# Performance work log

Measured on AMD Instinct MI355X. Metric: run time of the kernel, lower is better.

Reference implementation:

```python
import jax, jax.numpy as jnp
import numpy as np

N_QUBITS = 8
N_LAYERS = 3
BATCH = 8192


def setup_inputs() -> dict:
    key = jax.random.key(0)
    k0, k1, k2, k3 = jax.random.split(key, 4)
    return {
        "x": jax.random.normal(k0, (BATCH, N_QUBITS), jnp.float32),
        "quantum_weights": jax.random.normal(k1, (N_LAYERS, N_QUBITS, 2), jnp.float32) * 0.1,
        "W1": jax.random.normal(k2, (N_QUBITS, 64), jnp.float32) / np.float32(np.sqrt(N_QUBITS)),
        "b1": jnp.zeros((64,), jnp.float32),
        "W2": jax.random.normal(k3, (64, 256), jnp.float32) / np.float32(np.sqrt(64)),
        "b2": jnp.zeros((256,), jnp.float32),
    }


def _ry(theta):
    # RY(t) = [[cos t/2, -sin t/2], [sin t/2, cos t/2]]; theta: [] or [B]
    c = jnp.cos(theta * 0.5)
    s = jnp.sin(theta * 0.5)
    U = jnp.stack([jnp.stack([c, -s], axis=-1), jnp.stack([s, c], axis=-1)], axis=-2)
    return U.astype(jnp.complex64)


def _rz(theta):
    # RZ(t) = diag(e^{-it/2}, e^{it/2})
    em = jnp.exp(-0.5j * theta.astype(jnp.complex64))
    ep = jnp.exp(0.5j * theta.astype(jnp.complex64))
    z = jnp.zeros_like(em)
    return jnp.stack([jnp.stack([em, z], axis=-1), jnp.stack([z, ep], axis=-1)], axis=-2)


def _apply_1q(state, U, q):
    # state: [B, 2,2,...,2]; qubit q lives on axis q+1. U: [2,2] (shared) or [B,2,2].
    s = jnp.moveaxis(state, q + 1, -1)
    if U.ndim == 3:
        s = jnp.einsum('b...i,bji->b...j', s, U)
    else:
        s = jnp.einsum('b...i,ji->b...j', s, U)
    return jnp.moveaxis(s, -1, q + 1)


def _cnot(state, c, t):
    # flip target bit on the control=1 slice
    s = jnp.moveaxis(state, (c + 1, t + 1), (1, 2))
    s = jnp.stack([s[:, 0], s[:, 1, ::-1]], axis=1)
    return jnp.moveaxis(s, (1, 2), (c + 1, t + 1))


def _quantum_forward(x, qw):
    B = x.shape[0]
    xmin = x.min(axis=1, keepdims=True)
    xmax = x.max(axis=1, keepdims=True)
    xn = (x - xmin) / (xmax - xmin + 1e-8)
    # |0...0> state, shape [B, 2]*n
    state = jnp.zeros((B,) + (2,) * N_QUBITS, jnp.complex64)
    state = state.at[(slice(None),) + (0,) * N_QUBITS].set(1.0)
    # feature encoding: RY(x_norm * pi), per-sample angles
    for q in range(N_QUBITS):
        state = _apply_1q(state, _ry(xn[:, q] * jnp.pi), q)
    # variational layers
    for layer in range(N_LAYERS):
        for q in range(N_QUBITS):
            state = _apply_1q(state, _ry(qw[layer, q, 0]), q)
            state = _apply_1q(state, _rz(qw[layer, q, 1]), q)
        for q in range(N_QUBITS):
            state = _cnot(state, q, (q + 1) % N_QUBITS)
    probs = jnp.real(state * jnp.conj(state))  # [B, 2]*n, float32
    z = []
    for q in range(N_QUBITS):
        p = probs.sum(axis=tuple(a for a in range(1, N_QUBITS + 1) if a != q + 1))
        z.append(p[:, 0] - p[:, 1])  # <Z_q>
    return jnp.stack(z, axis=1)  # [B, n_qubits]


def reference(x, quantum_weights, W1, b1, W2, b2):
    z = _quantum_forward(x, quantum_weights).astype(jnp.float32)
    h = jax.nn.relu(z @ W1 + b1)
    return h @ W2 + b2
```

## Files before the change

### kernel.cpp

```cpp
#include <hip/hip_runtime.h>

#define NQ 8
#define NLAYERS 3

typedef unsigned int uint2ev __attribute__((ext_vector_type(2)));
typedef float f2 __attribute__((ext_vector_type(2)));
typedef __attribute__((address_space(3))) unsigned int lds_u32;
typedef __attribute__((address_space(1))) const unsigned int glb_u32;

template<int MASK>
__device__ __forceinline__ float xorlane(float v, int r) {
    if constexpr (MASK == 1) {
        return __int_as_float(__builtin_amdgcn_mov_dpp(__float_as_int(v), 0xB1, 0xF, 0xF, false));
    } else if constexpr (MASK == 2) {
        return __int_as_float(__builtin_amdgcn_mov_dpp(__float_as_int(v), 0x4E, 0xF, 0xF, false));
    } else if constexpr (MASK == 4) {
        return __int_as_float(__builtin_amdgcn_ds_swizzle(__float_as_int(v), 0x101F));
    } else if constexpr (MASK == 8) {
        return __int_as_float(__builtin_amdgcn_mov_dpp(__float_as_int(v), 0x128, 0xF, 0xF, false));
    }
}

template<int MASK>
__device__ __forceinline__ f2 xorlane2(f2 v, int r) {
    f2 o;
    o.x = xorlane<MASK>(v.x, r);
    o.y = xorlane<MASK>(v.y, r);
    return o;
}

template<int CTRL>
__device__ __forceinline__ float dpp_add_stage(float v) {
    int moved = __builtin_amdgcn_update_dpp(0, __float_as_int(v), CTRL, 0xF, 0xF, false);
    return v + __int_as_float(moved);
}
__device__ __forceinline__ float rowsum15(float v) {
    v = dpp_add_stage<0x111>(v);
    v = dpp_add_stage<0x112>(v);
    v = dpp_add_stage<0x114>(v);
    v = dpp_add_stage<0x118>(v);
    return v;
}

__device__ __forceinline__ float bcast15(float v) {
    return __int_as_float(__builtin_amdgcn_ds_swizzle(__float_as_int(v), 0x1F0));
}

__device__ __forceinline__ f2 cmul(f2 a, f2 b) {
    f2 r;
    r.x = a.x * b.x - a.y * b.y;
    r.y = a.x * b.y + a.y * b.x;
    return r;
}

__device__ __forceinline__ f2 splat(float c) { f2 v; v.x = c; v.y = c; return v; }

template<int Q>
__device__ __forceinline__ void ry16(float c, float s, f2 A[16], int r) {
    f2 vc = splat(c), vs = splat(s);
    if constexpr (Q < 4) {
        constexpr int M = 1 << Q;
#pragma unroll
        for (int j = 0; j < 16; ++j) if (!(j & M)) {
            f2 a0 = A[j], a1 = A[j | M];
            A[j]     = vc * a0 - vs * a1;
            A[j | M] = vs * a0 + vc * a1;
        }
    } else {
        constexpr int LM = 1 << (Q - 4);
        f2 vsg = (r & LM) ? vs : (splat(0.f) - vs);
#pragma unroll
        for (int j = 0; j < 16; ++j) {
            f2 p = xorlane2<LM>(A[j], r);
            A[j] = vc * A[j] + vsg * p;
        }
    }
}

__device__ __forceinline__ void ry16_q7_relab(float c, float s, f2 A[16], int r) {
    f2 vc = splat(c), vs = splat(s);
    f2 vsg = (r & 8) ? vs : (splat(0.f) - vs);
#pragma unroll
    for (int m = 0; m < 8; ++m) {
        f2 pa = xorlane2<8>(A[2 * m + 1], r);
        f2 pb = xorlane2<8>(A[2 * m],     r);
        A[2 * m]     = vc * A[2 * m]     + vsg * pa;
        A[2 * m + 1] = vc * A[2 * m + 1] + vsg * pb;
    }
}

__device__ __forceinline__ void ring16(f2 A[16], int lane, int r) {
    f2 t;
    t = A[1]; A[1] = A[3]; A[3] = t;
    t = A[5]; A[5] = A[7]; A[7] = t;
    t = A[9]; A[9] = A[11]; A[11] = t;
    t = A[13]; A[13] = A[15]; A[15] = t;
    t = A[2]; A[2] = A[6]; A[6] = t;
    t = A[3]; A[3] = A[7]; A[7] = t;
    t = A[10]; A[10] = A[14]; A[14] = t;
    t = A[11]; A[11] = A[15]; A[15] = t;
    t = A[4]; A[4] = A[12]; A[12] = t;
    t = A[5]; A[5] = A[13]; A[13] = t;
    t = A[6]; A[6] = A[14]; A[14] = t;
    t = A[7]; A[7] = A[15]; A[15] = t;

    int sA = ((lane & 48) | ((r ^ (r << 1)) & 15)) << 2;
    int sB = sA ^ 4;
#pragma unroll
    for (int j = 0; j < 8; ++j) {
        A[j].x = __int_as_float(__builtin_amdgcn_ds_bpermute(sA, __float_as_int(A[j].x)));
        A[j].y = __int_as_float(__builtin_amdgcn_ds_bpermute(sA, __float_as_int(A[j].y)));
    }
#pragma unroll
    for (int j = 8; j < 16; ++j) {
        A[j].x = __int_as_float(__builtin_amdgcn_ds_bpermute(sB, __float_as_int(A[j].x)));
        A[j].y = __int_as_float(__builtin_amdgcn_ds_bpermute(sB, __float_as_int(A[j].y)));
    }
}

__global__ __launch_bounds__(256) void qfused(
    const float* __restrict__ x,
    const float* __restrict__ qw,
    const float* __restrict__ W1,
    const float* __restrict__ b1,
    const float* __restrict__ W2,
    const float* __restrict__ b2,
    float* __restrict__ out,
    int B)
{
    __shared__ float4 tab[NLAYERS * NQ];
    __shared__ float h_lds[16][64];
    __shared__ float w2_lds[64 * 256];

    int tid = threadIdx.x;
    if (tid < NLAYERS * NQ) {
        float w0 = 0.5f * qw[tid * 2 + 0];
        float w1 = 0.5f * qw[tid * 2 + 1];
        if (tid < 8)
            tab[tid] = make_float4(w0, 0.f, __cosf(w1), __sinf(w1));
        else
            tab[tid] = make_float4(__cosf(w0), __sinf(w0), __cosf(w1), __sinf(w1));
    }

    int lane = tid & 63;
    int wid  = tid >> 6;
    int g    = lane >> 4;
    int r    = lane & 15;
    int sl   = wid * 4 + g;
    int sbase = blockIdx.x * 16;
    int sample = sbase + sl;
    if (sample >= B) sample = B - 1;

    const float4* x4 = (const float4*)(x + sample * 8);
    float4 xa = x4[0], xb = x4[1];

    __syncthreads();

#pragma unroll
    for (int k = 0; k < 16; ++k) {
        int row = wid * 16 + k;
        __builtin_amdgcn_global_load_lds(
            (glb_u32*)(W2 + row * 256 + lane * 4),
            (lds_u32*)&w2_lds[row * 256],
            16, 0, 0);
    }

    float xs[8] = {xa.x, xa.y, xa.z, xa.w, xb.x, xb.y, xb.z, xb.w};
    float xmin = xs[0], xmax = xs[0];
#pragma unroll
    for (int q = 1; q < 8; ++q) {
        xmin = fminf(xmin, xs[q]);
        xmax = fmaxf(xmax, xs[q]);
    }
    float inv_pi2 = 1.5707963267948966f / (xmax - xmin + 1e-8f);

    float4 T8 = tab[8],  T9 = tab[9],  T10 = tab[10], T11 = tab[11];
    float4 T12 = tab[12], T13 = tab[13], T14 = tab[14], T15 = tab[15];
    float4 T16 = tab[16], T17 = tab[17], T18 = tab[18], T19 = tab[19];
    float4 T20 = tab[20], T21 = tab[21], T22 = tab[22], T23 = tab[23];

    float cc[8], ss[8], cw[8], sw[8];
#pragma unroll
    for (int q = 0; q < 8; ++q) {
        float4 t0 = tab[q];
        float a = fmaf(xs[q] - xmin, inv_pi2, t0.x);
        __sincosf(a, &ss[q], &cc[q]);
        cw[q] = t0.z;
        sw[q] = t0.w;
    }

    int r0v = r & 1, r3v = (r >> 3) & 1;

    f2 X0[2], X1[2], X2[2], X3[2], X4[2];
#pragma unroll
    for (int k = 0; k < 2; ++k) {
        { int b = k ^ r3v; float rr = b ? ss[0] : cc[0];
          X0[k].x = rr * cw[0]; X0[k].y = (b ? rr : -rr) * sw[0]; }
        { int b = k ^ r3v; float rr = b ? ss[1] : cc[1];
          X1[k].x = rr * cw[1]; X1[k].y = (b ? rr : -rr) * sw[1]; }
        { int b = k;        float rr = b ? ss[2] : cc[2];
          X2[k].x = rr * cw[2]; X2[k].y = (b ? rr : -rr) * sw[2]; }
        { int b = k;        float rr = b ? ss[3] : cc[3];
          X3[k].x = rr * cw[3]; X3[k].y = (b ? rr : -rr) * sw[3]; }
        { int b = k ^ r0v;  float rr = b ? ss[4] : cc[4];
          X4[k].x = rr * cw[4]; X4[k].y = (b ? rr : -rr) * sw[4]; }
    }

    f2 pl;
    {
        int b5 = (r ^ (r >> 1)) & 1;
        int b6 = ((r >> 1) ^ (r >> 2)) & 1;
        int b7 = ((r >> 2) ^ (r >> 3)) & 1;
        f2 f5, f6, f7;
        float r5 = b5 ? ss[5] : cc[5];
        f5.x = r5 * cw[5]; f5.y = (b5 ? r5 : -r5) * sw[5];
        float r6 = b6 ? ss[6] : cc[6];
        f6.x = r6 * cw[6]; f6.y = (b6 ? r6 : -r6) * sw[6];
        float r7 = b7 ? ss[7] : cc[7];
        f7.x = r7 * cw[7]; f7.y = (b7 ? r7 : -r7) * sw[7];
        pl = cmul(cmul(f5, f6), f7);
    }

    f2 PP[2][2];
    {
        f2 t0 = cmul(pl, X0[0]);
        f2 t1 = cmul(pl, X0[1]);
        PP[0][0] = cmul(t0, X1[0]);
        PP[0][1] = cmul(t0, X1[1]);
        PP[1][0] = cmul(t1, X1[1]);
        PP[1][1] = cmul(t1, X1[0]);
    }
    f2 Q34[2][2];
    Q34[0][0] = cmul(X3[0], X4[0]);
    Q34[0][1] = cmul(X3[1], X4[1]);
    Q34[1][0] = cmul(X3[1], X4[0]);
    Q34[1][1] = cmul(X3[0], X4[1]);
    f2 R[2][2][2];
#pragma unroll
    for (int j1 = 0; j1 < 2; ++j1)
#pragma unroll
        for (int j2 = 0; j2 < 2; ++j2)
#pragma unroll
            for (int j3 = 0; j3 < 2; ++j3)
                R[j1][j2][j3] = cmul(X2[j1 ^ j2], Q34[j2][j3]);

    f2 A[16];
#pragma unroll
    for (int j3 = 0; j3 < 2; ++j3)
#pragma unroll
        for (int j2 = 0; j2 < 2; ++j2)
#pragma unroll
            for (int j1 = 0; j1 < 2; ++j1)
#pragma unroll
                for (int j0 = 0; j0 < 2; ++j0) {
                    int j = j0 + 2 * j1 + 4 * j2 + 8 * j3;
                    A[j] = cmul(PP[j0][j1], R[j1][j2][j3]);
                }

    ry16<0>(T8.x,  T8.y,  A, r);
    ry16<1>(T9.x,  T9.y,  A, r);
    ry16<2>(T10.x, T10.y, A, r);
    ry16<3>(T11.x, T11.y, A, r);
    ry16<4>(T12.x, T12.y, A, r);
    ry16<5>(T13.x, T13.y, A, r);
    ry16<6>(T14.x, T14.y, A, r);
    ry16<7>(T15.x, T15.y, A, r);

    {
        f2 L;
        {
            f2 d4, d5, d6, d7;
            d4.x = T12.z; d4.y = (r & 1) ? T12.w : -T12.w;
            d5.x = T13.z; d5.y = (r & 2) ? T13.w : -T13.w;
            d6.x = T14.z; d6.y = (r & 4) ? T14.w : -T14.w;
            d7.x = T15.z; d7.y = (r & 8) ? T15.w : -T15.w;
            L = cmul(cmul(d4, d5), cmul(d6, d7));
        }
        f2 d0n, d0p, d1n, d1p, d2n, d2p, d3n, d3p;
        d0n.x = T8.z;  d0n.y = -T8.w;   d0p.x = T8.z;  d0p.y = T8.w;
        d1n.x = T9.z;  d1n.y = -T9.w;   d1p.x = T9.z;  d1p.y = T9.w;
        d2n.x = T10.z; d2n.y = -T10.w;  d2p.x = T10.z; d2p.y = T10.w;
        d3n.x = T11.z; d3n.y = -T11.w;  d3p.x = T11.z; d3p.y = T11.w;

        f2 t01[4];
        {
            f2 l0 = cmul(L, d0n), l1 = cmul(L, d0p);
            t01[0] = cmul(l0, d1n);
            t01[1] = cmul(l1, d1n);
            t01[2] = cmul(l0, d1p);
            t01[3] = cmul(l1, d1p);
        }
        f2 m23[4];
        m23[0] = cmul(d2n, d3n);
        m23[1] = cmul(d2p, d3n);
        m23[2] = cmul(d2n, d3p);
        m23[3] = cmul(d2p, d3p);

#pragma unroll
        for (int j = 0; j < 16; ++j) {
            f2 D = cmul(t01[j & 3], m23[j >> 2]);
            A[j] = cmul(A[j], D);
        }
    }

    ring16(A, lane, r);

    {
        float s0l2 = (r & 8) ? -T16.y : T16.y;
        ry16<0>(T16.x, s0l2, A, r);
    }
    ry16<1>(T17.x, T17.y, A, r);
    ry16<2>(T18.x, T18.y, A, r);
    ry16<3>(T19.x, T19.y, A, r);
    ry16<4>(T20.x, T20.y, A, r);
    ry16<5>(T21.x, T21.y, A, r);
    ry16<6>(T22.x, T22.y, A, r);
    ry16_q7_relab(T23.x, T23.y, A, r);

    float P[16];
#pragma unroll
    for (int j = 0; j < 16; ++j) P[j] = A[j].x * A[j].x + A[j].y * A[j].y;

    float Sp[8], Dp[8];
#pragma unroll
    for (int k = 0; k < 8; ++k) {
        Sp[k] = P[2 * k] + P[2 * k + 1];
        Dp[k] = P[2 * k] - P[2 * k + 1];
    }
    float U0 = ((Sp[0] - Sp[1]) - (Sp[2] - Sp[3])) - ((Sp[4] - Sp[5]) - (Sp[6] - Sp[7]));
    float U3 = ((Dp[0] - Dp[1]) - (Dp[2] - Dp[3])) - ((Dp[4] - Dp[5]) - (Dp[6] - Dp[7]));
    float U1 = (Dp[0] - Dp[1]) + (Dp[2] - Dp[3]) + (Dp[4] - Dp[5]) + (Dp[6] - Dp[7]);
    float U2 = ((Dp[0] - Dp[1]) - (Dp[2] - Dp[3])) + ((Dp[4] - Dp[5]) - (Dp[6] - Dp[7]));

    {
        float sg73 = (r & 8) ? -1.f : 1.f;
        U1 *= sg73; U2 *= sg73; U3 *= sg73;
    }

    int p1 = r & 1;
    int p2 = (r ^ (r >> 1)) & 1;
    int p3 = (r ^ (r >> 1) ^ (r >> 2)) & 1;
    int p4 = (r ^ (r >> 1) ^ (r >> 2) ^ (r >> 3)) & 1;

    float z0 = bcast15(rowsum15(p4 ? -U0 : U0));
    float z1 = bcast15(rowsum15(U1));
    float z2 = bcast15(rowsum15(U2));
    float z3 = bcast15(rowsum15(U3));
    float z4 = bcast15(rowsum15(p1 ? -U3 : U3));
    float z5 = bcast15(rowsum15(p2 ? -U3 : U3));
    float z6 = bcast15(rowsum15(p3 ? -U3 : U3));
    float z7 = bcast15(rowsum15(p4 ? -U3 : U3));

    {
        int c0 = r * 4;
        f2 accL = *(const f2*)(b1 + c0);
        f2 accH = *(const f2*)(b1 + c0 + 2);
        const float* w1p = W1 + c0;
        float zq[8] = {z0, z1, z2, z3, z4, z5, z6, z7};
#pragma unroll
        for (int q = 0; q < 8; ++q) {
            f2 wL = *(const f2*)(w1p + q * 64);
            f2 wH = *(const f2*)(w1p + q * 64 + 2);
            f2 zz = splat(zq[q]);
            accL = accL + zz * wL;
            accH = accH + zz * wH;
        }
        accL.x = fmaxf(accL.x, 0.f); accL.y = fmaxf(accL.y, 0.f);
        accH.x = fmaxf(accH.x, 0.f); accH.y = fmaxf(accH.y, 0.f);
        *(float4*)&h_lds[sl][c0] = make_float4(accL.x, accL.y, accH.x, accH.y);
    }
    __syncthreads();

    int sg = tid >> 6;
    int c4 = (tid & 63) * 4;
    f2 bbL = *(const f2*)(b2 + c4);
    f2 bbH = *(const f2*)(b2 + c4 + 2);
    f2 a0L = bbL, a0H = bbH, a1L = bbL, a1H = bbH;
    f2 a2L = bbL, a2H = bbH, a3L = bbL, a3H = bbH;
    const int sO = sg * 4;

#pragma unroll 2
    for (int i4 = 0; i4 < 16; ++i4) {
        const float* wrow = &w2_lds[i4 * 4 * 256 + c4];
        f2 w0L = *(const f2*)(wrow);        f2 w0H = *(const f2*)(wrow + 2);
        f2 w1L = *(const f2*)(wrow + 256);  f2 w1H = *(const f2*)(wrow + 258);
        f2 w2L = *(const f2*)(wrow + 512);  f2 w2H = *(const f2*)(wrow + 514);
        f2 w3L = *(const f2*)(wrow + 768);  f2 w3H = *(const f2*)(wrow + 770);
        float4 h0 = *(const float4*)&h_lds[sO + 0][i4 * 4];
        float4 h1 = *(const float4*)&h_lds[sO + 1][i4 * 4];
        float4 h2 = *(const float4*)&h_lds[sO + 2][i4 * 4];
        float4 h3 = *(const float4*)&h_lds[sO + 3][i4 * 4];

        a0L = a0L + splat(h0.x) * w0L + splat(h0.y) * w1L + splat(h0.z) * w2L + splat(h0.w) * w3L;
        a0H = a0H + splat(h0.x) * w0H + splat(h0.y) * w1H + splat(h0.z) * w2H + splat(h0.w) * w3H;
        a1L = a1L + splat(h1.x) * w0L + splat(h1.y) * w1L + splat(h1.z) * w2L + splat(h1.w) * w3L;
        a1H = a1H + splat(h1.x) * w0H + splat(h1.y) * w1H + splat(h1.z) * w2H + splat(h1.w) * w3H;
        a2L = a2L + splat(h2.x) * w0L + splat(h2.y) * w1L + splat(h2.z) * w2L + splat(h2.w) * w3L;
        a2H = a2H + splat(h2.x) * w0H + splat(h2.y) * w1H + splat(h2.z) * w2H + splat(h2.w) * w3H;
        a3L = a3L + splat(h3.x) * w0L + splat(h3.y) * w1L + splat(h3.z) * w2L + splat(h3.w) * w3L;
        a3H = a3H + splat(h3.x) * w0H + splat(h3.y) * w1H + splat(h3.z) * w2H + splat(h3.w) * w3H;
    }

    int srow = sbase + sO;
    if (srow + 0 < B) *(float4*)(out + (srow + 0) * 256 + c4) = make_float4(a0L.x, a0L.y, a0H.x, a0H.y);
    if (srow + 1 < B) *(float4*)(out + (srow + 1) * 256 + c4) = make_float4(a1L.x, a1L.y, a1H.x, a1H.y);
    if (srow + 2 < B) *(float4*)(out + (srow + 2) * 256 + c4) = make_float4(a2L.x, a2L.y, a2H.x, a2H.y);
    if (srow + 3 < B) *(float4*)(out + (srow + 3) * 256 + c4) = make_float4(a3L.x, a3L.y, a3H.x, a3H.y);
}

extern "C" void kernel_launch(void* const* d_in, const int* in_sizes, int n_in,
                              void* d_out, int out_size, void* d_ws, size_t ws_size,
                              hipStream_t stream) {
    const float* x  = (const float*)d_in[0];
    const float* qw = (const float*)d_in[1];
    const float* W1 = (const float*)d_in[2];
    const float* b1 = (const float*)d_in[3];
    const float* W2 = (const float*)d_in[4];
    const float* b2 = (const float*)d_in[5];
    float* out = (float*)d_out;

    int B = in_sizes[0] / NQ;

    qfused<<<(B + 15) / 16, 256, 0, stream>>>(x, qw, W1, b1, W2, b2, out, B);
}
```

Before: 17.97 us.

## Process two samples per 16-lane group and halve block size to 128 threads

Each 16-lane group now simulates two samples' statevectors interleaved, so the block needs 128 threads instead of 256 while still covering 16 samples. The state-building, rotation, measurement and dense layers are factored into helpers called twice, which gives more instruction-level parallelism per thread. Each thread's W2 LDS load count doubles and the second GEMM accumulates 8 rows per thread. The cost is higher register pressure and fewer waves per block, which may reduce latency hiding.

After: 19.57 us. +8.9%, slower.

```diff
diff --git a/kernel.cpp b/kernel.cpp
--- a/kernel.cpp
+++ b/kernel.cpp
@@ -118,7 +118,168 @@
     }
 }
 
-__global__ __launch_bounds__(256) void qfused(
+__device__ __forceinline__ void build_state(const float xs[8], const float4* tab,
+                                            int r, f2 A[16]) {
+    float xmin = xs[0], xmax = xs[0];
+#pragma unroll
+    for (int q = 1; q < 8; ++q) {
+        xmin = fminf(xmin, xs[q]);
+        xmax = fmaxf(xmax, xs[q]);
+    }
+    float inv_pi2 = 1.5707963267948966f / (xmax - xmin + 1e-8f);
+
+    float cc[8], ss[8], cw[8], sw[8];
+#pragma unroll
+    for (int q = 0; q < 8; ++q) {
+        float4 t0 = tab[q];
+        float a = fmaf(xs[q] - xmin, inv_pi2, t0.x);
+        __sincosf(a, &ss[q], &cc[q]);
+        cw[q] = t0.z;
+        sw[q] = t0.w;
+    }
+
+    int r0v = r & 1, r3v = (r >> 3) & 1;
+
+    f2 X0[2], X1[2], X2[2], X3[2], X4[2];
+#pragma unroll
+    for (int k = 0; k < 2; ++k) {
+        { int b = k ^ r3v; float rr = b ? ss[0] : cc[0];
+          X0[k].x = rr * cw[0]; X0[k].y = (b ? rr : -rr) * sw[0]; }
+        { int b = k ^ r3v; float rr = b ? ss[1] : cc[1];
+          X1[k].x = rr * cw[1]; X1[k].y = (b ? rr : -rr) * sw[1]; }
+        { int b = k;        float rr = b ? ss[2] : cc[2];
+          X2[k].x = rr * cw[2]; X2[k].y = (b ? rr : -rr) * sw[2]; }
+        { int b = k;        float rr = b ? ss[3] : cc[3];
+          X3[k].x = rr * cw[3]; X3[k].y = (b ? rr : -rr) * sw[3]; }
+        { int b = k ^ r0v;  float rr = b ? ss[4] : cc[4];
+          X4[k].x = rr * cw[4]; X4[k].y = (b ? rr : -rr) * sw[4]; }
+    }
+
+    f2 pl;
+    {
+        int b5 = (r ^ (r >> 1)) & 1;
+        int b6 = ((r >> 1) ^ (r >> 2)) & 1;
+        int b7 = ((r >> 2) ^ (r >> 3)) & 1;
+        f2 f5, f6, f7;
+        float r5 = b5 ? ss[5] : cc[5];
+        f5.x = r5 * cw[5]; f5.y = (b5 ? r5 : -r5) * sw[5];
+        float r6 = b6 ? ss[6] : cc[6];
+        f6.x = r6 * cw[6]; f6.y = (b6 ? r6 : -r6) * sw[6];
+        float r7 = b7 ? ss[7] : cc[7];
+        f7.x = r7 * cw[7]; f7.y = (b7 ? r7 : -r7) * sw[7];
+        pl = cmul(cmul(f5, f6), f7);
+    }
+
+    f2 PP[2][2];
+    {
+        f2 t0 = cmul(pl, X0[0]);
+        f2 t1 = cmul(pl, X0[1]);
+        PP[0][0] = cmul(t0, X1[0]);
+        PP[0][1] = cmul(t0, X1[1]);
+        PP[1][0] = cmul(t1, X1[1]);
+        PP[1][1] = cmul(t1, X1[0]);
+    }
+    f2 Q34[2][2];
+    Q34[0][0] = cmul(X3[0], X4[0]);
+    Q34[0][1] = cmul(X3[1], X4[1]);
+    Q34[1][0] = cmul(X3[1], X4[0]);
+    Q34[1][1] = cmul(X3[0], X4[1]);
+    f2 R[2][2][2];
+#pragma unroll
+    for (int j1 = 0; j1 < 2; ++j1)
+#pragma unroll
+        for (int j2 = 0; j2 < 2; ++j2)
+#pragma unroll
+            for (int j3 = 0; j3 < 2; ++j3)
+                R[j1][j2][j3] = cmul(X2[j1 ^ j2], Q34[j2][j3]);
+
+#pragma unroll
+    for (int j3 = 0; j3 < 2; ++j3)
+#pragma unroll
+        for (int j2 = 0; j2 < 2; ++j2)
+#pragma unroll
+            for (int j1 = 0; j1 < 2; ++j1)
+#pragma unroll
+                for (int j0 = 0; j0 < 2; ++j0) {
+                    int j = j0 + 2 * j1 + 4 * j2 + 8 * j3;
+                    A[j] = cmul(PP[j0][j1], R[j1][j2][j3]);
+                }
+}
+
+__device__ __forceinline__ void rz1_diag(const float4* tab, int r, f2 A[16]) {
+    float4 T12 = tab[12], T13 = tab[13], T14 = tab[14], T15 = tab[15];
+    float4 T8 = tab[8], T9 = tab[9], T10 = tab[10], T11 = tab[11];
+    f2 L;
+    {
+        f2 d4, d5, d6, d7;
+        d4.x = T12.z; d4.y = (r & 1) ? T12.w : -T12.w;
+        d5.x = T13.z; d5.y = (r & 2) ? T13.w : -T13.w;
+        d6.x = T14.z; d6.y = (r & 4) ? T14.w : -T14.w;
+        d7.x = T15.z; d7.y = (r & 8) ? T15.w : -T15.w;
+        L = cmul(cmul(d4, d5), cmul(d6, d7));
+    }
+    f2 d0n, d0p, d1n, d1p, d2n, d2p, d3n, d3p;
+    d0n.x = T8.z;  d0n.y = -T8.w;   d0p.x = T8.z;  d0p.y = T8.w;
+    d1n.x = T9.z;  d1n.y = -T9.w;   d1p.x = T9.z;  d1p.y = T9.w;
+    d2n.x = T10.z; d2n.y = -T10.w;  d2p.x = T10.z; d2p.y = T10.w;
+    d3n.x = T11.z; d3n.y = -T11.w;  d3p.x = T11.z; d3p.y = T11.w;
+
+    f2 t01[4];
+    {
+        f2 l0 = cmul(L, d0n), l1 = cmul(L, d0p);
+        t01[0] = cmul(l0, d1n);
+        t01[1] = cmul(l1, d1n);
+        t01[2] = cmul(l0, d1p);
+        t01[3] = cmul(l1, d1p);
+    }
+    f2 m23[4];
+    m23[0] = cmul(d2n, d3n);
+    m23[1] = cmul(d2p, d3n);
+    m23[2] = cmul(d2n, d3p);
+    m23[3] = cmul(d2p, d3p);
+
+#pragma unroll
+    for (int j = 0; j < 16; ++j) {
+        f2 D = cmul(t01[j & 3], m23[j >> 2]);
+        A[j] = cmul(A[j], D);
+    }
+}
+
+__device__ __forceinline__ void measure16(const f2 A[16], int r, float z[8]) {
+    float P[16];
+#pragma unroll
+    for (int j = 0; j < 16; ++j) P[j] = A[j].x * A[j].x + A[j].y * A[j].y;
+
+    float Sp[8], Dp[8];
+#pragma unroll
+    for (int k = 0; k < 8; ++k) {
+        Sp[k] = P[2 * k] + P[2 * k + 1];
+        Dp[k] = P[2 * k] - P[2 * k + 1];
+    }
+    float U0 = ((Sp[0] - Sp[1]) - (Sp[2] - Sp[3])) - ((Sp[4] - Sp[5]) - (Sp[6] - Sp[7]));
+    float U3 = ((Dp[0] - Dp[1]) - (Dp[2] - Dp[3])) - ((Dp[4] - Dp[5]) - (Dp[6] - Dp[7]));
+    float U1 = (Dp[0] - Dp[1]) + (Dp[2] - Dp[3]) + (Dp[4] - Dp[5]) + (Dp[6] - Dp[7]);
+    float U2 = ((Dp[0] - Dp[1]) - (Dp[2] - Dp[3])) + ((Dp[4] - Dp[5]) - (Dp[6] - Dp[7]));
+
+    float sg73 = (r & 8) ? -1.f : 1.f;
+    U1 *= sg73; U2 *= sg73; U3 *= sg73;
+
+    int p1 = r & 1;
+    int p2 = (r ^ (r >> 1)) & 1;
+    int p3 = (r ^ (r >> 1) ^ (r >> 2)) & 1;
+    int p4 = (r ^ (r >> 1) ^ (r >> 2) ^ (r >> 3)) & 1;
+
+    z[0] = bcast15(rowsum15(p4 ? -U0 : U0));
+    z[1] = bcast15(rowsum15(U1));
+    z[2] = bcast15(rowsum15(U2));
+    z[3] = bcast15(rowsum15(U3));
+    z[4] = bcast15(rowsum15(p1 ? -U3 : U3));
+    z[5] = bcast15(rowsum15(p2 ? -U3 : U3));
+    z[6] = bcast15(rowsum15(p3 ? -U3 : U3));
+    z[7] = bcast15(rowsum15(p4 ? -U3 : U3));
+}
+
+__global__ __launch_bounds__(128) void qfused(
     const float* __restrict__ x,
     const float* __restrict__ qw,
     const float* __restrict__ W1,
@@ -146,238 +307,105 @@
     int wid  = tid >> 6;
     int g    = lane >> 4;
     int r    = lane & 15;
-    int sl   = wid * 4 + g;
+    int slA  = wid * 8 + g;
+    int slB  = slA + 4;
     int sbase = blockIdx.x * 16;
-    int sample = sbase + sl;
-    if (sample >= B) sample = B - 1;
-
-    const float4* x4 = (const float4*)(x + sample * 8);
-    float4 xa = x4[0], xb = x4[1];
+    int sampleA = sbase + slA; if (sampleA >= B) sampleA = B - 1;
+    int sampleB = sbase + slB; if (sampleB >= B) sampleB = B - 1;
+
+    const float4* xA4 = (const float4*)(x + sampleA * 8);
+    float4 xa0 = xA4[0], xa1 = xA4[1];
+    const float4* xB4 = (const float4*)(x + sampleB * 8);
+    float4 xb0 = xB4[0], xb1 = xB4[1];
 
     __syncthreads();
 
 #pragma unroll
-    for (int k = 0; k < 16; ++k) {
-        int row = wid * 16 + k;
+    for (int k = 0; k < 32; ++k) {
+        int row = wid * 32 + k;
         __builtin_amdgcn_global_load_lds(
             (glb_u32*)(W2 + row * 256 + lane * 4),
             (lds_u32*)&w2_lds[row * 256],
             16, 0, 0);
     }
 
-    float xs[8] = {xa.x, xa.y, xa.z, xa.w, xb.x, xb.y, xb.z, xb.w};
-    float xmin = xs[0], xmax = xs[0];
-#pragma unroll
-    for (int q = 1; q < 8; ++q) {
-        xmin = fminf(xmin, xs[q]);
-        xmax = fmaxf(xmax, xs[q]);
-    }
-    float inv_pi2 = 1.5707963267948966f / (xmax - xmin + 1e-8f);
-
-    float4 T8 = tab[8],  T9 = tab[9],  T10 = tab[10], T11 = tab[11];
-    float4 T12 = tab[12], T13 = tab[13], T14 = tab[14], T15 = tab[15];
-    float4 T16 = tab[16], T17 = tab[17], T18 = tab[18], T19 = tab[19];
-    float4 T20 = tab[20], T21 = tab[21], T22 = tab[22], T23 = tab[23];
-
-    float cc[8], ss[8], cw[8], sw[8];
-#pragma unroll
-    for (int q = 0; q < 8; ++q) {
-        float4 t0 = tab[q];
-        float a = fmaf(xs[q] - xmin, inv_pi2, t0.x);
-        __sincosf(a, &ss[q], &cc[q]);
-        cw[q] = t0.z;
-        sw[q] = t0.w;
-    }
-
-    int r0v = r & 1, r3v = (r >> 3) & 1;
-
-    f2 X0[2], X1[2], X2[2], X3[2], X4[2];
-#pragma unroll
-    for (int k = 0; k < 2; ++k) {
-        { int b = k ^ r3v; float rr = b ? ss[0] : cc[0];
-          X0[k].x = rr * cw[0]; X0[k].y = (b ? rr : -rr) * sw[0]; }
-        { int b = k ^ r3v; float rr = b ? ss[1] : cc[1];
-          X1[k].x = rr * cw[1]; X1[k].y = (b ? rr : -rr) * sw[1]; }
-        { int b = k;        float rr = b ? ss[2] : cc[2];
-          X2[k].x = rr * cw[2]; X2[k].y = (b ? rr : -rr) * sw[2]; }
-        { int b = k;        float rr = b ? ss[3] : cc[3];
-          X3[k].x = rr * cw[3]; X3[k].y = (b ? rr : -rr) * sw[3]; }
-        { int b = k ^ r0v;  float rr = b ? ss[4] : cc[4];
-          X4[k].x = rr * cw[4]; X4[k].y = (b ? rr : -rr) * sw[4]; }
-    }
-
-    f2 pl;
-    {
-        int b5 = (r ^ (r >> 1)) & 1;
-        int b6 = ((r >> 1) ^ (r >> 2)) & 1;
-        int b7 = ((r >> 2) ^ (r >> 3)) & 1;
-        f2 f5, f6, f7;
-        float r5 = b5 ? ss[5] : cc[5];
-        f5.x = r5 * cw[5]; f5.y = (b5 ? r5 : -r5) * sw[5];
-        float r6 = b6 ? ss[6] : cc[6];
-        f6.x = r6 * cw[6]; f6.y = (b6 ? r6 : -r6) * sw[6];
-        float r7 = b7 ? ss[7] : cc[7];
-        f7.x = r7 * cw[7]; f7.y = (b7 ? r7 : -r7) * sw[7];
-        pl = cmul(cmul(f5, f6), f7);
-    }
-
-    f2 PP[2][2];
-    {
-        f2 t0 = cmul(pl, X0[0]);
-        f2 t1 = cmul(pl, X0[1]);
-        PP[0][0] = cmul(t0, X1[0]);
-        PP[0][1] = cmul(t0, X1[1]);
-        PP[1][0] = cmul(t1, X1[1]);
-        PP[1][1] = cmul(t1, X1[0]);
-    }
-    f2 Q34[2][2];
-    Q34[0][0] = cmul(X3[0], X4[0]);
-    Q34[0][1] = cmul(X3[1], X4[1]);
-    Q34[1][0] = cmul(X3[1], X4[0]);
-    Q34[1][1] = cmul(X3[0], X4[1]);
-    f2 R[2][2][2];
-#pragma unroll
-    for (int j1 = 0; j1 < 2; ++j1)
-#pragma unroll
-        for (int j2 = 0; j2 < 2; ++j2)
-#pragma unroll
-            for (int j3 = 0; j3 < 2; ++j3)
-                R[j1][j2][j3] = cmul(X2[j1 ^ j2], Q34[j2][j3]);
-
-    f2 A[16];
-#pragma unroll
-    for (int j3 = 0; j3 < 2; ++j3)
-#pragma unroll
-        for (int j2 = 0; j2 < 2; ++j2)
-#pragma unroll
-            for (int j1 = 0; j1 < 2; ++j1)
-#pragma unroll
-                for (int j0 = 0; j0 < 2; ++j0) {
-                    int j = j0 + 2 * j1 + 4 * j2 + 8 * j3;
-                    A[j] = cmul(PP[j0][j1], R[j1][j2][j3]);
-                }
-
-    ry16<0>(T8.x,  T8.y,  A, r);
-    ry16<1>(T9.x,  T9.y,  A, r);
-    ry16<2>(T10.x, T10.y, A, r);
-    ry16<3>(T11.x, T11.y, A, r);
-    ry16<4>(T12.x, T12.y, A, r);
-    ry16<5>(T13.x, T13.y, A, r);
-    ry16<6>(T14.x, T14.y, A, r);
-    ry16<7>(T15.x, T15.y, A, r);
-
-    {
-        f2 L;
-        {
-            f2 d4, d5, d6, d7;
-            d4.x = T12.z; d4.y = (r & 1) ? T12.w : -T12.w;
-            d5.x = T13.z; d5.y = (r & 2) ? T13.w : -T13.w;
-            d6.x = T14.z; d6.y = (r & 4) ? T14.w : -T14.w;
-            d7.x = T15.z; d7.y = (r & 8) ? T15.w : -T15.w;
-            L = cmul(cmul(d4, d5), cmul(d6, d7));
-        }
-        f2 d0n, d0p, d1n, d1p, d2n, d2p, d3n, d3p;
-        d0n.x = T8.z;  d0n.y = -T8.w;   d0p.x = T8.z;  d0p.y = T8.w;
-        d1n.x = T9.z;  d1n.y = -T9.w;   d1p.x = T9.z;  d1p.y = T9.w;
-        d2n.x = T10.z; d2n.y = -T10.w;  d2p.x = T10.z; d2p.y = T10.w;
-        d3n.x = T11.z; d3n.y = -T11.w;  d3p.x = T11.z; d3p.y = T11.w;
-
-        f2 t01[4];
-        {
-            f2 l0 = cmul(L, d0n), l1 = cmul(L, d0p);
-            t01[0] = cmul(l0, d1n);
-            t01[1] = cmul(l1, d1n);
-            t01[2] = cmul(l0, d1p);
-            t01[3] = cmul(l1, d1p);
-        }
-        f2 m23[4];
-        m23[0] = cmul(d2n, d3n);
-        m23[1] = cmul(d2p, d3n);
-        m23[2] = cmul(d2n, d3p);
-        m23[3] = cmul(d2p, d3p);
-
-#pragma unroll
-        for (int j = 0; j < 16; ++j) {
-            f2 D = cmul(t01[j & 3], m23[j >> 2]);
-            A[j] = cmul(A[j], D);
-        }
-    }
-
-    ring16(A, lane, r);
-
-    {
-        float s0l2 = (r & 8) ? -T16.y : T16.y;
-        ry16<0>(T16.x, s0l2, A, r);
-    }
-    ry16<1>(T17.x, T17.y, A, r);
-    ry16<2>(T18.x, T18.y, A, r);
-    ry16<3>(T19.x, T19.y, A, r);
-    ry16<4>(T20.x, T20.y, A, r);
-    ry16<5>(T21.x, T21.y, A, r);
-    ry16<6>(T22.x, T22.y, A, r);
-    ry16_q7_relab(T23.x, T23.y, A, r);
-
-    float P[16];
-#pragma unroll
-    for (int j = 0; j < 16; ++j) P[j] = A[j].x * A[j].x + A[j].y * A[j].y;
-
-    float Sp[8], Dp[8];
-#pragma unroll
-    for (int k = 0; k < 8; ++k) {
-        Sp[k] = P[2 * k] + P[2 * k + 1];
-        Dp[k] = P[2 * k] - P[2 * k + 1];
-    }
-    float U0 = ((Sp[0] - Sp[1]) - (Sp[2] - Sp[3])) - ((Sp[4] - Sp[5]) - (Sp[6] - Sp[7]));
-    float U3 = ((Dp[0] - Dp[1]) - (Dp[2] - Dp[3])) - ((Dp[4] - Dp[5]) - (Dp[6] - Dp[7]));
-    float U1 = (Dp[0] - Dp[1]) + (Dp[2] - Dp[3]) + (Dp[4] - Dp[5]) + (Dp[6] - Dp[7]);
-    float U2 = ((Dp[0] - Dp[1]) - (Dp[2] - Dp[3])) + ((Dp[4] - Dp[5]) - (Dp[6] - Dp[7]));
-
-    {
-        float sg73 = (r & 8) ? -1.f : 1.f;
-        U1 *= sg73; U2 *= sg73; U3 *= sg73;
-    }
-
-    int p1 = r & 1;
-    int p2 = (r ^ (r >> 1)) & 1;
-    int p3 = (r ^ (r >> 1) ^ (r >> 2)) & 1;
-    int p4 = (r ^ (r >> 1) ^ (r >> 2) ^ (r >> 3)) & 1;
-
-    float z0 = bcast15(rowsum15(p4 ? -U0 : U0));
-    float z1 = bcast15(rowsum15(U1));
-    float z2 = bcast15(rowsum15(U2));
-    float z3 = bcast15(rowsum15(U3));
-    float z4 = bcast15(rowsum15(p1 ? -U3 : U3));
-    float z5 = bcast15(rowsum15(p2 ? -U3 : U3));
-    float z6 = bcast15(rowsum15(p3 ? -U3 : U3));
-    float z7 = bcast15(rowsum15(p4 ? -U3 : U3));
+    float xsA[8] = {xa0.x, xa0.y, xa0.z, xa0.w, xa1.x, xa1.y, xa1.z, xa1.w};
+    float xsB[8] = {xb0.x, xb0.y, xb0.z, xb0.w, xb1.x, xb1.y, xb1.z, xb1.w};
+
+    f2 SA[16], SB[16];
+    build_state(xsA, tab, r, SA);
+    build_state(xsB, tab, r, SB);
+
+    {
+        float4 t;
+        t = tab[8];  ry16<0>(t.x, t.y, SA, r); ry16<0>(t.x, t.y, SB, r);
+        t = tab[9];  ry16<1>(t.x, t.y, SA, r); ry16<1>(t.x, t.y, SB, r);
+        t = tab[10]; ry16<2>(t.x, t.y, SA, r); ry16<2>(t.x, t.y, SB, r);
+        t = tab[11]; ry16<3>(t.x, t.y, SA, r); ry16<3>(t.x, t.y, SB, r);
+        t = tab[12]; ry16<4>(t.x, t.y, SA, r); ry16<4>(t.x, t.y, SB, r);
+        t = tab[13]; ry16<5>(t.x, t.y, SA, r); ry16<5>(t.x, t.y, SB, r);
+        t = tab[14]; ry16<6>(t.x, t.y, SA, r); ry16<6>(t.x, t.y, SB, r);
+        t = tab[15]; ry16<7>(t.x, t.y, SA, r); ry16<7>(t.x, t.y, SB, r);
+    }
+
+    rz1_diag(tab, r, SA);
+    rz1_diag(tab, r, SB);
+
+    ring16(SA, lane, r);
+    ring16(SB, lane, r);
+
+    {
+        float4 t = tab[16];
+        float s0l2 = (r & 8) ? -t.y : t.y;
+        ry16<0>(t.x, s0l2, SA, r); ry16<0>(t.x, s0l2, SB, r);
+    }
+    {
+        float4 t;
+        t = tab[17]; ry16<1>(t.x, t.y, SA, r); ry16<1>(t.x, t.y, SB, r);
+        t = tab[18]; ry16<2>(t.x, t.y, SA, r); ry16<2>(t.x, t.y, SB, r);
+        t = tab[19]; ry16<3>(t.x, t.y, SA, r); ry16<3>(t.x, t.y, SB, r);
+        t = tab[20]; ry16<4>(t.x, t.y, SA, r); ry16<4>(t.x, t.y, SB, r);
+        t = tab[21]; ry16<5>(t.x, t.y, SA, r); ry16<5>(t.x, t.y, SB, r);
+        t = tab[22]; ry16<6>(t.x, t.y, SA, r); ry16<6>(t.x, t.y, SB, r);
+        t = tab[23]; ry16_q7_relab(t.x, t.y, SA, r); ry16_q7_relab(t.x, t.y, SB, r);
+    }
+
+    float zA[8], zB[8];
+    measure16(SA, r, zA);
+    measure16(SB, r, zB);
 
     {
         int c0 = r * 4;
-        f2 accL = *(const f2*)(b1 + c0);
-        f2 accH = *(const f2*)(b1 + c0 + 2);
         const float* w1p = W1 + c0;
-        float zq[8] = {z0, z1, z2, z3, z4, z5, z6, z7};
+        f2 aAL = *(const f2*)(b1 + c0);
+        f2 aAH = *(const f2*)(b1 + c0 + 2);
+        f2 aBL = aAL, aBH = aAH;
 #pragma unroll
         for (int q = 0; q < 8; ++q) {
             f2 wL = *(const f2*)(w1p + q * 64);
             f2 wH = *(const f2*)(w1p + q * 64 + 2);
-            f2 zz = splat(zq[q]);
-            accL = accL + zz * wL;
-            accH = accH + zz * wH;
+            aAL = aAL + splat(zA[q]) * wL;
+            aAH = aAH + splat(zA[q]) * wH;
+            aBL = aBL + splat(zB[q]) * wL;
+            aBH = aBH + splat(zB[q]) * wH;
         }
-        accL.x = fmaxf(accL.x, 0.f); accL.y = fmaxf(accL.y, 0.f);
-        accH.x = fmaxf(accH.x, 0.f); accH.y = fmaxf(accH.y, 0.f);
-        *(float4*)&h_lds[sl][c0] = make_float4(accL.x, accL.y, accH.x, accH.y);
+        aAL.x = fmaxf(aAL.x, 0.f); aAL.y = fmaxf(aAL.y, 0.f);
+        aAH.x = fmaxf(aAH.x, 0.f); aAH.y = fmaxf(aAH.y, 0.f);
+        aBL.x = fmaxf(aBL.x, 0.f); aBL.y = fmaxf(aBL.y, 0.f);
+        aBH.x = fmaxf(aBH.x, 0.f); aBH.y = fmaxf(aBH.y, 0.f);
+        *(float4*)&h_lds[slA][c0] = make_float4(aAL.x, aAL.y, aAH.x, aAH.y);
+        *(float4*)&h_lds[slB][c0] = make_float4(aBL.x, aBL.y, aBH.x, aBH.y);
     }
     __syncthreads();
 
     int sg = tid >> 6;
     int c4 = (tid & 63) * 4;
+    int sO = sg * 8;
     f2 bbL = *(const f2*)(b2 + c4);
     f2 bbH = *(const f2*)(b2 + c4 + 2);
-    f2 a0L = bbL, a0H = bbH, a1L = bbL, a1H = bbH;
-    f2 a2L = bbL, a2H = bbH, a3L = bbL, a3H = bbH;
-    const int sO = sg * 4;
+    f2 aL[8], aH[8];
+#pragma unroll
+    for (int s = 0; s < 8; ++s) { aL[s] = bbL; aH[s] = bbH; }
 
 #pragma unroll 2
     for (int i4 = 0; i4 < 16; ++i4) {
@@ -386,26 +414,21 @@
         f2 w1L = *(const f2*)(wrow + 256);  f2 w1H = *(const f2*)(wrow + 258);
         f2 w2L = *(const f2*)(wrow + 512);  f2 w2H = *(const f2*)(wrow + 514);
         f2 w3L = *(const f2*)(wrow + 768);  f2 w3H = *(const f2*)(wrow + 770);
-        float4 h0 = *(const float4*)&h_lds[sO + 0][i4 * 4];
-        float4 h1 = *(const float4*)&h_lds[sO + 1][i4 * 4];
-        float4 h2 = *(const float4*)&h_lds[sO + 2][i4 * 4];
-        float4 h3 = *(const float4*)&h_lds[sO + 3][i4 * 4];
-
-        a0L = a0L + splat(h0.x) * w0L + splat(h0.y) * w1L + splat(h0.z) * w2L + splat(h0.w) * w3L;
-        a0H = a0H + splat(h0.x) * w0H + splat(h0.y) * w1H + splat(h0.z) * w2H + splat(h0.w) * w3H;
-        a1L = a1L + splat(h1.x) * w0L + splat(h1.y) * w1L + splat(h1.z) * w2L + splat(h1.w) * w3L;
-        a1H = a1H + splat(h1.x) * w0H + splat(h1.y) * w1H + splat(h1.z) * w2H + splat(h1.w) * w3H;
-        a2L = a2L + splat(h2.x) * w0L + splat(h2.y) * w1L + splat(h2.z) * w2L + splat(h2.w) * w3L;
-        a2H = a2H + splat(h2.x) * w0H + splat(h2.y) * w1H + splat(h2.z) * w2H + splat(h2.w) * w3H;
-        a3L = a3L + splat(h3.x) * w0L + splat(h3.y) * w1L + splat(h3.z) * w2L + splat(h3.w) * w3L;
-        a3H = a3H + splat(h3.x) * w0H + splat(h3.y) * w1H + splat(h3.z) * w2H + splat(h3.w) * w3H;
+#pragma unroll
+        for (int s = 0; s < 8; ++s) {
+            float4 h4 = *(const float4*)&h_lds[sO + s][i4 * 4];
+            aL[s] = aL[s] + splat(h4.x) * w0L + splat(h4.y) * w1L + splat(h4.z) * w2L + splat(h4.w) * w3L;
+            aH[s] = aH[s] + splat(h4.x) * w0H + splat(h4.y) * w1H + splat(h4.z) * w2H + splat(h4.w) * w3H;
+        }
     }
 
     int srow = sbase + sO;
-    if (srow + 0 < B) *(float4*)(out + (srow + 0) * 256 + c4) = make_float4(a0L.x, a0L.y, a0H.x, a0H.y);
-    if (srow + 1 < B) *(float4*)(out + (srow + 1) * 256 + c4) = make_float4(a1L.x, a1L.y, a1H.x, a1H.y);
-    if (srow + 2 < B) *(float4*)(out + (srow + 2) * 256 + c4) = make_float4(a2L.x, a2L.y, a2H.x, a2H.y);
-    if (srow + 3 < B) *(float4*)(out + (srow + 3) * 256 + c4) = make_float4(a3L.x, a3L.y, a3H.x, a3H.y);
+#pragma unroll
+    for (int s = 0; s < 8; ++s) {
+        if (srow + s < B)
+            *(float4*)(out + (srow + s) * 256 + c4) =
+                make_float4(aL[s].x, aL[s].y, aH[s].x, aH[s].y);
+    }
 }
 
 extern "C" void kernel_launch(void* const* d_in, const int* in_sizes, int n_in,
@@ -421,5 +444,5 @@
 
     int B = in_sizes[0] / NQ;
 
-    qfused<<<(B + 15) / 16, 256, 0, stream>>>(x, qw, W1, b1, W2, b2, out, B);
-}
+    qfused<<<(B + 15) / 16, 128, 0, stream>>>(x, qw, W1, b1, W2, b2, out, B);
+}
```
